# Kernel tuning notes

Measured on AMD Instinct MI355X. Metric: run time of the kernel, lower is better.

## Reference

```python
import jax, jax.numpy as jnp
import numpy as np

LEN_HIS = 20   # q_len_his: sliding-window history length
DIM_C = 4      # dim_c
H = 64         # GRU hidden = final_mlp_hidden_width
D = 36         # global_graph_width(32) + goal(2) + action(2)
N = 32768      # total timesteps across many episodes


def setup_inputs() -> dict:
    key = jax.random.key(0)
    ks = jax.random.split(key, 8)
    emb = jax.random.normal(ks[0], (N, D), jnp.float32)
    dones = (jax.random.uniform(ks[1], (N, 1)) < 0.02).astype(jnp.int32)
    s = lambda k, shape, fan: jax.random.normal(k, shape, jnp.float32) / np.sqrt(fan).astype(np.float32)
    return {
        "embeddings": emb,
        "W_ih": s(ks[2], (3 * H, D), D),
        "W_hh": s(ks[3], (3 * H, H), H),
        "b_ih": jnp.zeros((3 * H,), jnp.float32),
        "b_hh": jnp.zeros((3 * H,), jnp.float32),
        "W1": s(ks[4], (H, H), H),
        "b1": jnp.zeros((H,), jnp.float32),
        "W2": s(ks[5], (DIM_C, H), H),
        "b2": jnp.zeros((DIM_C,), jnp.float32),
        "dones": dones,
    }


def _his_calculate_c(embeddings, W_ih, W_hh, b_ih, b_hh, W1, b1, W2, b2, dones):
    """Batched/padded version of the ragged sliding-window GRU+MLP loop.

    For each timestep t, the torch code runs the GRU over
    embeddings[max(episode_start, t-L+1) : t+1] from a zero hidden state,
    then applies FinalPredMLP to the final hidden state.
    """
    n = embeddings.shape[0]
    done = dones[:, 0] != 0
    idx = jnp.arange(n)
    # episode_start[t] = (index of most recent done strictly before t) + 1, else 0
    prev_done = jnp.concatenate([jnp.zeros((1,), bool), done[:-1]])
    ep_start = jax.lax.cummax(jnp.where(prev_done, idx, 0))
    win_start = jnp.maximum(ep_start, idx - LEN_HIS + 1)            # [N]

    # padded windows: position l holds embeddings[t - (L-1) + l]
    gidx = idx[:, None] - (LEN_HIS - 1) + jnp.arange(LEN_HIS)[None, :]  # [N, L]
    valid = gidx >= win_start[:, None]                                   # [N, L]
    X = embeddings[jnp.clip(gidx, 0, n - 1)] * valid[..., None]          # [N, L, D]

    def cell(h, inp):
        x, v = inp                      # x: [N, D], v: [N]
        gi = x @ W_ih.T + b_ih          # [N, 3H]
        gh = h @ W_hh.T + b_hh          # [N, 3H]
        ir, iz, inn = jnp.split(gi, 3, axis=-1)
        hr, hz, hnn = jnp.split(gh, 3, axis=-1)
        r = jax.nn.sigmoid(ir + hr)
        z = jax.nn.sigmoid(iz + hz)
        ncand = jnp.tanh(inn + r * hnn)
        h_new = (1.0 - z) * ncand + z * h
        return jnp.where(v[:, None], h_new, h), None

    h0 = jnp.zeros((n, H), embeddings.dtype)
    hT, _ = jax.lax.scan(cell, h0, (jnp.swapaxes(X, 0, 1), valid.T))  # [N, H]

    # FinalPredMLP: Linear(H,H) -> ReLU -> Linear(H, dim_c)
    hid = jax.nn.relu(hT @ W1.T + b1)
    return hid @ W2.T + b2              # [N, dim_c]


def reference(embeddings, W_ih, W_hh, b_ih, b_hh, W1, b1, W2, b2, dones):
    return _his_calculate_c(embeddings, W_ih, W_hh, b_ih, b_hh, W1, b1, W2, b2, dones)
```

## Files before the change

kernel.cpp:

```cpp
#include <hip/hip_runtime.h>

#define NT 32768
#define DI 36
#define HH 64
#define G3 192
#define LH 20
#define SGS 196

#define NLOG2E -1.4426950408889634f
#define TLOG2E 2.8853900817779268f

#define UNION_OFF  27440
#define SFIRST_OFF 32480
#define SMEM_BYTES 32544

typedef __attribute__((ext_vector_type(8))) short bf16x8;
typedef __attribute__((ext_vector_type(4))) float f32x4;
typedef __attribute__((ext_vector_type(4))) int int4v;
union frag_cast { int4v i4; bf16x8 h8; };

__device__ __forceinline__ unsigned f2u(float f) { union { float f; unsigned u; } x; x.f = f; return x.u; }
__device__ __forceinline__ float u2f(unsigned u) { union { float f; unsigned u; } x; x.u = u; return x.f; }
__device__ __forceinline__ unsigned short f2bf_rne(float f) {
    union { float f; unsigned u; } x; x.f = f;
    unsigned r = x.u + 0x7FFFu + ((x.u >> 16) & 1u);
    return (unsigned short)(r >> 16);
}

__global__ __launch_bounds__(64) void prep_kernel(
    const float* __restrict__ W_ih, const float* __restrict__ W_hh,
    const float* __restrict__ W1, int4v* __restrict__ wfrag)
{
    const int b = (int)blockIdx.x;
    const int l = (int)threadIdx.x;
    unsigned short e[8];
    if (b < 72) {
        const int set = b / 24, fb = b % 24;
        const int mt = fb >> 1, kt = fb & 1;
        const int m = mt * 16 + (l & 15);
        const float sc = ((mt >> 2) < 2) ? NLOG2E : TLOG2E;
        const int k0 = kt * 32 + (l >> 4) * 8;
#pragma unroll
        for (int jj = 0; jj < 8; ++jj) {
            const int k = k0 + jj;
            if (set == 2) {
                e[jj] = f2bf_rne(W_hh[(size_t)m * HH + k] * sc);
            } else {
                const float v = (k < DI) ? W_ih[(size_t)m * DI + k] * sc : 0.f;
                const unsigned u = f2u(v);
                if (set == 0) e[jj] = (unsigned short)(u >> 16);
                else          e[jj] = (unsigned short)(f2u(v - u2f(u & 0xFFFF0000u)) >> 16);
            }
        }
    } else {
        const int bb = b - 72;
        const bool is_lo = bb >= 8;
        const int f = bb & 7;
        const int mt = f >> 1, kt = f & 1;
        const int m = mt * 16 + (l & 15);
        const int k0 = kt * 32 + (l >> 4) * 8;
#pragma unroll
        for (int jj = 0; jj < 8; ++jj) {
            const float v = W1[(size_t)m * HH + k0 + jj];
            const unsigned u = f2u(v);
            if (!is_lo) e[jj] = (unsigned short)(u >> 16);
            else        e[jj] = (unsigned short)(f2u(v - u2f(u & 0xFFFF0000u)) >> 16);
        }
    }
    int4v p;
    p.x = e[0] | ((unsigned)e[1] << 16); p.y = e[2] | ((unsigned)e[3] << 16);
    p.z = e[4] | ((unsigned)e[5] << 16); p.w = e[6] | ((unsigned)e[7] << 16);
    wfrag[b * 64 + l] = p;
}

__global__ __launch_bounds__(256, 5) void gru_kernel(
    const float* __restrict__ emb, const int4v* __restrict__ wfrag,
    const float* __restrict__ b_ih, const float* __restrict__ b_hh,
    const float* __restrict__ b1, const float* __restrict__ W2,
    const float* __restrict__ b2, const int* __restrict__ dones,
    float* __restrict__ out)
{
    __shared__ __align__(16) char SMEM[SMEM_BYTES];
    float* const Sg = (float*)SMEM;
    unsigned short* const EmbP = (unsigned short*)(SMEM + UNION_OFF);
    unsigned short* const HbB  = (unsigned short*)(SMEM + UNION_OFF);
    unsigned short* const HfH  = (unsigned short*)(SMEM + UNION_OFF);
    unsigned short* const HfL  = HfH + 1152;
    int* const sfirst = (int*)(SMEM + SFIRST_OFF);

    const int tid = threadIdx.x;
    const int lane = tid & 63;
    const int W = tid >> 6;
    const int li = lane & 15;
    const int q = lane >> 4;
    const int blk = ((int)blockIdx.x & 7) * 256 + ((int)blockIdx.x >> 3);
    const int T0 = blk * 16;

    float ev[5];
#pragma unroll
    for (int k = 0; k < 5; ++k) {
        const int i = tid + 256 * k;
        if (i < 35 * DI) {
            const int r = i / DI, c = i % DI;
            int tt = T0 - (LH - 1) + r; tt = tt < 0 ? 0 : tt;
            ev[k] = emb[(size_t)tt * DI + c];
        }
    }
    {
        int4v* z = (int4v*)EmbP;
        for (int i = tid; i < 315; i += 256) z[i] = int4v{0, 0, 0, 0};
    }
    if (tid < 16) {
        const int tt = T0 + tid;
        int lo = tt - (LH - 1); if (lo < 0) lo = 0;
        int ws = lo;
        for (int j = lo; j < tt; ++j)
            ws = (dones[j] != 0) ? (j + 1) : ws;
        sfirst[tid] = ws - (tt - (LH - 1));
    }
    __syncthreads();
#pragma unroll
    for (int k = 0; k < 5; ++k) {
        const int i = tid + 256 * k;
        if (i < 35 * DI)
            EmbP[(i / DI) * 72 + (i % DI)] = (unsigned short)(f2u(ev[k]) >> 16);
    }

    bf16x8 aih[3][2], ail[3][2];
#pragma unroll
    for (int g = 0; g < 3; ++g)
#pragma unroll
        for (int kt = 0; kt < 2; ++kt) {
            const int fb = (4 * g + W) * 2 + kt;
            frag_cast a, b;
            a.i4 = wfrag[(0 * 24 + fb) * 64 + lane];
            b.i4 = wfrag[(1 * 24 + fb) * 64 + lane];
            aih[g][kt] = a.h8; ail[g][kt] = b.h8;
        }

    const int joff = 16 * W + 4 * q;
    f32x4 biasI[3];
#pragma unroll
    for (int g = 0; g < 3; ++g) {
        const float sc = (g < 2) ? NLOG2E : TLOG2E;
        const f32x4 bi = *(const f32x4*)&b_ih[64 * g + joff];
        if (g < 2) {
            const f32x4 bh = *(const f32x4*)&b_hh[64 * g + joff];
#pragma unroll
            for (int rr = 0; rr < 4; ++rr) biasI[g][rr] = (bi[rr] + bh[rr]) * sc;
        } else {
#pragma unroll
            for (int rr = 0; rr < 4; ++rr) biasI[g][rr] = bi[rr] * sc;
        }
    }
    __syncthreads();

#pragma unroll
    for (int nt = 0; nt < 3; ++nt) {
        const int row = 16 * nt + li;
        const int rowr = row < 35 ? row : 34;
        bf16x8 ebh[2];
#pragma unroll
        for (int kt = 0; kt < 2; ++kt)
            ebh[kt] = *(const bf16x8*)&EmbP[rowr * 72 + 32 * kt + 8 * q];
#pragma unroll
        for (int g = 0; g < 3; ++g) {
            f32x4 a = biasI[g];
            a = __builtin_amdgcn_mfma_f32_16x16x32_bf16(aih[g][0], ebh[0], a, 0, 0, 0);
            a = __builtin_amdgcn_mfma_f32_16x16x32_bf16(aih[g][1], ebh[1], a, 0, 0, 0);
            a = __builtin_amdgcn_mfma_f32_16x16x32_bf16(ail[g][0], ebh[0], a, 0, 0, 0);
            a = __builtin_amdgcn_mfma_f32_16x16x32_bf16(ail[g][1], ebh[1], a, 0, 0, 0);
            if (row < 35)
                *(f32x4*)&Sg[row * SGS + 64 * g + joff] = a;
        }
    }
    __syncthreads();
#pragma unroll
    for (int k = 0; k < 5; ++k) {
        const int i = tid + 256 * k;
        if (i < 35 * DI) {
            const unsigned u = f2u(ev[k]);
            EmbP[(i / DI) * 72 + (i % DI)] =
                (unsigned short)(f2u(ev[k] - u2f(u & 0xFFFF0000u)) >> 16);
        }
    }
    __syncthreads();

#pragma unroll
    for (int nt = 0; nt < 3; ++nt) {
        const int row = 16 * nt + li;
        const int rowr = row < 35 ? row : 34;
        bf16x8 ebl[2];
#pragma unroll
        for (int kt = 0; kt < 2; ++kt)
            ebl[kt] = *(const bf16x8*)&EmbP[rowr * 72 + 32 * kt + 8 * q];
#pragma unroll
        for (int g = 0; g < 3; ++g) {
            f32x4 a = *(const f32x4*)&Sg[rowr * SGS + 64 * g + joff];
            a = __builtin_amdgcn_mfma_f32_16x16x32_bf16(aih[g][0], ebl[0], a, 0, 0, 0);
            a = __builtin_amdgcn_mfma_f32_16x16x32_bf16(aih[g][1], ebl[1], a, 0, 0, 0);
            if (row < 35)
                *(f32x4*)&Sg[row * SGS + 64 * g + joff] = a;
        }
    }
    __syncthreads();
    const int sfr = sfirst[li];

    bf16x8 whh[3][2];
#pragma unroll
    for (int g = 0; g < 3; ++g)
#pragma unroll
        for (int kt = 0; kt < 2; ++kt) {
            frag_cast c; c.i4 = wfrag[(48 + (4 * g + W) * 2 + kt) * 64 + lane];
            whh[g][kt] = c.h8;
        }
    f32x4 bnv;
    {
        const f32x4 b = *(const f32x4*)&b_hh[128 + joff];
#pragma unroll
        for (int rr = 0; rr < 4; ++rr) bnv[rr] = b[rr] * TLOG2E;
    }

    float h[4] = {0.f, 0.f, 0.f, 0.f};
    f32x4 accR, accZ, accN, ginv;
    f32x4 gvR, gvZ, gvN;

    {
        const float* gp = Sg + li * SGS;
        accR = *(const f32x4*)(gp + joff);
        accZ = *(const f32x4*)(gp + 64 + joff);
        ginv = *(const f32x4*)(gp + 128 + joff);
        accN = bnv;
        const bool valid = (0 >= sfr);
#pragma unroll
        for (int rr = 0; rr < 4; ++rr) {
            const float r  = __builtin_amdgcn_rcpf(1.f + __builtin_amdgcn_exp2f(accR[rr]));
            const float z  = __builtin_amdgcn_rcpf(1.f + __builtin_amdgcn_exp2f(accZ[rr]));
            const float nc = 1.f - 2.f * __builtin_amdgcn_rcpf(1.f + __builtin_amdgcn_exp2f(ginv[rr] + r * accN[rr]));
            h[rr] = valid ? fmaf(z, 0.f - nc, nc) : 0.f;
        }
        uint2 ph;
        ph.x = __builtin_amdgcn_perm(f2u(h[1]), f2u(h[0]), 0x07060302u);
        ph.y = __builtin_amdgcn_perm(f2u(h[3]), f2u(h[2]), 0x07060302u);
        *(uint2*)&HbB[1152 + li * 72 + joff] = ph;
        const float* gq = Sg + (li + 1) * SGS;
        gvR = *(const f32x4*)(gq + joff);
        gvZ = *(const f32x4*)(gq + 64 + joff);
        gvN = *(const f32x4*)(gq + 128 + joff);
    }
    __syncthreads();

#pragma unroll 2
    for (int s = 1; s < LH; ++s) {
        const int rb = s & 1;
        const bf16x8 bh0 = *(const bf16x8*)&HbB[rb * 1152 + li * 72 + 8 * q];
        const bf16x8 bh1 = *(const bf16x8*)&HbB[rb * 1152 + li * 72 + 32 + 8 * q];

        accR = gvR; accZ = gvZ; ginv = gvN; accN = bnv;
        {
            int r = li + s + 1; r = r > 34 ? 34 : r;
            const float* gq = Sg + r * SGS;
            gvR = *(const f32x4*)(gq + joff);
            gvZ = *(const f32x4*)(gq + 64 + joff);
            gvN = *(const f32x4*)(gq + 128 + joff);
        }
#pragma unroll
        for (int g = 0; g < 3; ++g) {
            f32x4 a = (g == 0) ? accR : (g == 1) ? accZ : accN;
            a = __builtin_amdgcn_mfma_f32_16x16x32_bf16(whh[g][0], bh0, a, 0, 0, 0);
            a = __builtin_amdgcn_mfma_f32_16x16x32_bf16(whh[g][1], bh1, a, 0, 0, 0);
            if (g == 0) accR = a; else if (g == 1) accZ = a; else accN = a;
        }
        const bool valid = (s >= sfr);
#pragma unroll
        for (int rr = 0; rr < 4; ++rr) {
            const float r  = __builtin_amdgcn_rcpf(1.f + __builtin_amdgcn_exp2f(accR[rr]));
            const float z  = __builtin_amdgcn_rcpf(1.f + __builtin_amdgcn_exp2f(accZ[rr]));
            const float nc = 1.f - 2.f * __builtin_amdgcn_rcpf(1.f + __builtin_amdgcn_exp2f(ginv[rr] + r * accN[rr]));
            const float hn = fmaf(z, h[rr] - nc, nc);
            h[rr] = valid ? hn : h[rr];
        }
        if (s != LH - 1) {
            uint2 ph;
            ph.x = __builtin_amdgcn_perm(f2u(h[1]), f2u(h[0]), 0x07060302u);
            ph.y = __builtin_amdgcn_perm(f2u(h[3]), f2u(h[2]), 0x07060302u);
            *(uint2*)&HbB[(1 - rb) * 1152 + li * 72 + joff] = ph;
        }
        __syncthreads();
    }

    {
        const unsigned u0 = f2u(h[0]), u1 = f2u(h[1]);
        const unsigned u2 = f2u(h[2]), u3 = f2u(h[3]);
        uint2 ph, pl;
        ph.x = __builtin_amdgcn_perm(u1, u0, 0x07060302u);
        ph.y = __builtin_amdgcn_perm(u3, u2, 0x07060302u);
        const unsigned l0 = f2u(h[0] - u2f(u0 & 0xFFFF0000u));
        const unsigned l1 = f2u(h[1] - u2f(u1 & 0xFFFF0000u));
        const unsigned l2 = f2u(h[2] - u2f(u2 & 0xFFFF0000u));
        const unsigned l3 = f2u(h[3] - u2f(u3 & 0xFFFF0000u));
        pl.x = __builtin_amdgcn_perm(l1, l0, 0x07060302u);
        pl.y = __builtin_amdgcn_perm(l3, l2, 0x07060302u);
        *(uint2*)&HfH[li * 72 + joff] = ph;
        *(uint2*)&HfL[li * 72 + joff] = pl;
    }
    __syncthreads();
    {
        bf16x8 w1h[2], w1l[2];
#pragma unroll
        for (int kt = 0; kt < 2; ++kt) {
            frag_cast a, b;
            a.i4 = wfrag[(72 + W * 2 + kt) * 64 + lane];
            b.i4 = wfrag[(80 + W * 2 + kt) * 64 + lane];
            w1h[kt] = a.h8; w1l[kt] = b.h8;
        }
        const bf16x8 bh0 = *(const bf16x8*)&HfH[li * 72 + 8 * q];
        const bf16x8 bh1 = *(const bf16x8*)&HfH[li * 72 + 32 + 8 * q];
        const bf16x8 bl0 = *(const bf16x8*)&HfL[li * 72 + 8 * q];
        const bf16x8 bl1 = *(const bf16x8*)&HfL[li * 72 + 32 + 8 * q];
        f32x4 a = *(const f32x4*)&b1[joff];
        a = __builtin_amdgcn_mfma_f32_16x16x32_bf16(w1h[0], bh0, a, 0, 0, 0);
        a = __builtin_amdgcn_mfma_f32_16x16x32_bf16(w1h[1], bh1, a, 0, 0, 0);
        a = __builtin_amdgcn_mfma_f32_16x16x32_bf16(w1l[0], bh0, a, 0, 0, 0);
        a = __builtin_amdgcn_mfma_f32_16x16x32_bf16(w1l[1], bh1, a, 0, 0, 0);
        a = __builtin_amdgcn_mfma_f32_16x16x32_bf16(w1h[0], bl0, a, 0, 0, 0);
        a = __builtin_amdgcn_mfma_f32_16x16x32_bf16(w1h[1], bl1, a, 0, 0, 0);
        __syncthreads();
        float4 st;
        st.x = fmaxf(a[0], 0.f); st.y = fmaxf(a[1], 0.f);
        st.z = fmaxf(a[2], 0.f); st.w = fmaxf(a[3], 0.f);
        *(float4*)&Sg[li * 68 + joff] = st;
    }
    __syncthreads();
    if (tid < 64) {
        const int tt = tid >> 2, c = tid & 3;
        float o2 = b2[c];
        for (int m4 = 0; m4 < 16; ++m4) {
            const float4 hv = *(const float4*)&Sg[tt * 68 + 4 * m4];
            const float4 wv = *(const float4*)&W2[c * HH + 4 * m4];
            o2 += hv.x * wv.x + hv.y * wv.y + hv.z * wv.z + hv.w * wv.w;
        }
        out[(size_t)(T0 + tt) * 4 + c] = o2;
    }
}

extern "C" void kernel_launch(void* const* d_in, const int* in_sizes, int n_in,
                              void* d_out, int out_size, void* d_ws, size_t ws_size,
                              hipStream_t stream) {
    const float* emb  = (const float*)d_in[0];
    const float* W_ih = (const float*)d_in[1];
    const float* W_hh = (const float*)d_in[2];
    const float* b_ih = (const float*)d_in[3];
    const float* b_hh = (const float*)d_in[4];
    const float* W1   = (const float*)d_in[5];
    const float* b1   = (const float*)d_in[6];
    const float* W2   = (const float*)d_in[7];
    const float* b2   = (const float*)d_in[8];
    const int*   dn   = (const int*)d_in[9];

    int4v* wfrag = (int4v*)d_ws;
    float* o = (float*)d_out;

    prep_kernel<<<88, 64, 0, stream>>>(W_ih, W_hh, W1, wfrag);
    gru_kernel<<<NT / 16, 256, 0, stream>>>(emb, wfrag, b_ih, b_hh,
                                            b1, W2, b2, dn, o);
}
```

Before: 116.9 us.

## Store input-gate preactivations as fp16 in LDS and merge embedding split passes

```diff
diff --git a/kernel.cpp b/kernel.cpp
--- a/kernel.cpp
+++ b/kernel.cpp
@@ -1,18 +1,19 @@
 #include <hip/hip_runtime.h>
+#include <hip/hip_fp16.h>
 
 #define NT 32768
 #define DI 36
 #define HH 64
 #define G3 192
 #define LH 20
-#define SGS 196
+#define SGH 200
 
 #define NLOG2E -1.4426950408889634f
 #define TLOG2E 2.8853900817779268f
 
-#define UNION_OFF  27440
-#define SFIRST_OFF 32480
-#define SMEM_BYTES 32544
+#define UNION_OFF  14000
+#define SFIRST_OFF 24080
+#define SMEM_BYTES 24144
 
 typedef __attribute__((ext_vector_type(8))) short bf16x8;
 typedef __attribute__((ext_vector_type(4))) float f32x4;
@@ -25,6 +26,17 @@
     union { float f; unsigned u; } x; x.f = f;
     unsigned r = x.u + 0x7FFFu + ((x.u >> 16) & 1u);
     return (unsigned short)(r >> 16);
+}
+__device__ __forceinline__ f32x4 h4f(uint2 p) {
+    const __half2* a = (const __half2*)&p;
+    const float2 f0 = __half22float2(a[0]);
+    const float2 f1 = __half22float2(a[1]);
+    f32x4 r; r[0] = f0.x; r[1] = f0.y; r[2] = f1.x; r[3] = f1.y; return r;
+}
+__device__ __forceinline__ uint2 f4h(f32x4 v) {
+    __half2 h0 = __floats2half2_rn(v[0], v[1]);
+    __half2 h1 = __floats2half2_rn(v[2], v[3]);
+    uint2 r; r.x = *(unsigned*)&h0; r.y = *(unsigned*)&h1; return r;
 }
 
 __global__ __launch_bounds__(64) void prep_kernel(
@@ -73,7 +85,7 @@
     wfrag[b * 64 + l] = p;
 }
 
-__global__ __launch_bounds__(256, 5) void gru_kernel(
+__global__ __launch_bounds__(256, 6) void gru_kernel(
     const float* __restrict__ emb, const int4v* __restrict__ wfrag,
     const float* __restrict__ b_ih, const float* __restrict__ b_hh,
     const float* __restrict__ b1, const float* __restrict__ W2,
@@ -81,8 +93,9 @@
     float* __restrict__ out)
 {
     __shared__ __align__(16) char SMEM[SMEM_BYTES];
-    float* const Sg = (float*)SMEM;
-    unsigned short* const EmbP = (unsigned short*)(SMEM + UNION_OFF);
+    unsigned short* const Sg = (unsigned short*)SMEM;
+    unsigned short* const EmbH = (unsigned short*)(SMEM + UNION_OFF);
+    unsigned short* const EmbL = EmbH + 35 * 72;
     unsigned short* const HbB  = (unsigned short*)(SMEM + UNION_OFF);
     unsigned short* const HfH  = (unsigned short*)(SMEM + UNION_OFF);
     unsigned short* const HfL  = HfH + 1152;
@@ -107,8 +120,8 @@
         }
     }
     {
-        int4v* z = (int4v*)EmbP;
-        for (int i = tid; i < 315; i += 256) z[i] = int4v{0, 0, 0, 0};
+        int4v* z = (int4v*)EmbH;
+        for (int i = tid; i < 630; i += 256) z[i] = int4v{0, 0, 0, 0};
     }
     if (tid < 16) {
         const int tt = T0 + tid;
@@ -122,8 +135,12 @@
 #pragma unroll
     for (int k = 0; k < 5; ++k) {
         const int i = tid + 256 * k;
-        if (i < 35 * DI)
-            EmbP[(i / DI) * 72 + (i % DI)] = (unsigned short)(f2u(ev[k]) >> 16);
+        if (i < 35 * DI) {
+            const int idx = (i / DI) * 72 + (i % DI);
+            const unsigned u = f2u(ev[k]);
+            EmbH[idx] = (unsigned short)(u >> 16);
+            EmbL[idx] = (unsigned short)(f2u(ev[k] - u2f(u & 0xFFFF0000u)) >> 16);
+        }
     }
 
     bf16x8 aih[3][2], ail[3][2];
@@ -159,10 +176,12 @@
     for (int nt = 0; nt < 3; ++nt) {
         const int row = 16 * nt + li;
         const int rowr = row < 35 ? row : 34;
-        bf16x8 ebh[2];
-#pragma unroll
-        for (int kt = 0; kt < 2; ++kt)
-            ebh[kt] = *(const bf16x8*)&EmbP[rowr * 72 + 32 * kt + 8 * q];
+        bf16x8 ebh[2], ebl[2];
+#pragma unroll
+        for (int kt = 0; kt < 2; ++kt) {
+            ebh[kt] = *(const bf16x8*)&EmbH[rowr * 72 + 32 * kt + 8 * q];
+            ebl[kt] = *(const bf16x8*)&EmbL[rowr * 72 + 32 * kt + 8 * q];
+        }
 #pragma unroll
         for (int g = 0; g < 3; ++g) {
             f32x4 a = biasI[g];
@@ -170,37 +189,10 @@
             a = __builtin_amdgcn_mfma_f32_16x16x32_bf16(aih[g][1], ebh[1], a, 0, 0, 0);
             a = __builtin_amdgcn_mfma_f32_16x16x32_bf16(ail[g][0], ebh[0], a, 0, 0, 0);
             a = __builtin_amdgcn_mfma_f32_16x16x32_bf16(ail[g][1], ebh[1], a, 0, 0, 0);
-            if (row < 35)
-                *(f32x4*)&Sg[row * SGS + 64 * g + joff] = a;
-        }
-    }
-    __syncthreads();
-#pragma unroll
-    for (int k = 0; k < 5; ++k) {
-        const int i = tid + 256 * k;
-        if (i < 35 * DI) {
-            const unsigned u = f2u(ev[k]);
-            EmbP[(i / DI) * 72 + (i % DI)] =
-                (unsigned short)(f2u(ev[k] - u2f(u & 0xFFFF0000u)) >> 16);
-        }
-    }
-    __syncthreads();
-
-#pragma unroll
-    for (int nt = 0; nt < 3; ++nt) {
-        const int row = 16 * nt + li;
-        const int rowr = row < 35 ? row : 34;
-        bf16x8 ebl[2];
-#pragma unroll
-        for (int kt = 0; kt < 2; ++kt)
-            ebl[kt] = *(const bf16x8*)&EmbP[rowr * 72 + 32 * kt + 8 * q];
-#pragma unroll
-        for (int g = 0; g < 3; ++g) {
-            f32x4 a = *(const f32x4*)&Sg[rowr * SGS + 64 * g + joff];
             a = __builtin_amdgcn_mfma_f32_16x16x32_bf16(aih[g][0], ebl[0], a, 0, 0, 0);
             a = __builtin_amdgcn_mfma_f32_16x16x32_bf16(aih[g][1], ebl[1], a, 0, 0, 0);
             if (row < 35)
-                *(f32x4*)&Sg[row * SGS + 64 * g + joff] = a;
+                *(uint2*)&Sg[row * SGH + 64 * g + joff] = f4h(a);
         }
     }
     __syncthreads();
@@ -223,13 +215,12 @@
 
     float h[4] = {0.f, 0.f, 0.f, 0.f};
     f32x4 accR, accZ, accN, ginv;
-    f32x4 gvR, gvZ, gvN;
-
-    {
-        const float* gp = Sg + li * SGS;
-        accR = *(const f32x4*)(gp + joff);
-        accZ = *(const f32x4*)(gp + 64 + joff);
-        ginv = *(const f32x4*)(gp + 128 + joff);
+    uint2 pR, pZ, pN;
+
+    {
+        accR = h4f(*(const uint2*)&Sg[li * SGH + joff]);
+        accZ = h4f(*(const uint2*)&Sg[li * SGH + 64 + joff]);
+        ginv = h4f(*(const uint2*)&Sg[li * SGH + 128 + joff]);
         accN = bnv;
         const bool valid = (0 >= sfr);
 #pragma unroll
@@ -243,10 +234,9 @@
         ph.x = __builtin_amdgcn_perm(f2u(h[1]), f2u(h[0]), 0x07060302u);
         ph.y = __builtin_amdgcn_perm(f2u(h[3]), f2u(h[2]), 0x07060302u);
         *(uint2*)&HbB[1152 + li * 72 + joff] = ph;
-        const float* gq = Sg + (li + 1) * SGS;
-        gvR = *(const f32x4*)(gq + joff);
-        gvZ = *(const f32x4*)(gq + 64 + joff);
-        gvN = *(const f32x4*)(gq + 128 + joff);
+        pR = *(const uint2*)&Sg[(li + 1) * SGH + joff];
+        pZ = *(const uint2*)&Sg[(li + 1) * SGH + 64 + joff];
+        pN = *(const uint2*)&Sg[(li + 1) * SGH + 128 + joff];
     }
     __syncthreads();
 
@@ -256,13 +246,12 @@
         const bf16x8 bh0 = *(const bf16x8*)&HbB[rb * 1152 + li * 72 + 8 * q];
         const bf16x8 bh1 = *(const bf16x8*)&HbB[rb * 1152 + li * 72 + 32 + 8 * q];
 
-        accR = gvR; accZ = gvZ; ginv = gvN; accN = bnv;
+        accR = h4f(pR); accZ = h4f(pZ); ginv = h4f(pN); accN = bnv;
         {
             int r = li + s + 1; r = r > 34 ? 34 : r;
-            const float* gq = Sg + r * SGS;
-            gvR = *(const f32x4*)(gq + joff);
-            gvZ = *(const f32x4*)(gq + 64 + joff);
-            gvN = *(const f32x4*)(gq + 128 + joff);
+            pR = *(const uint2*)&Sg[r * SGH + joff];
+            pZ = *(const uint2*)&Sg[r * SGH + 64 + joff];
+            pN = *(const uint2*)&Sg[r * SGH + 128 + joff];
         }
 #pragma unroll
         for (int g = 0; g < 3; ++g) {
@@ -305,6 +294,7 @@
         *(uint2*)&HfL[li * 72 + joff] = pl;
     }
     __syncthreads();
+    float* const Hid = (float*)SMEM;
     {
         bf16x8 w1h[2], w1l[2];
 #pragma unroll
@@ -329,14 +319,14 @@
         float4 st;
         st.x = fmaxf(a[0], 0.f); st.y = fmaxf(a[1], 0.f);
         st.z = fmaxf(a[2], 0.f); st.w = fmaxf(a[3], 0.f);
-        *(float4*)&Sg[li * 68 + joff] = st;
+        *(float4*)&Hid[li * 68 + joff] = st;
     }
     __syncthreads();
     if (tid < 64) {
         const int tt = tid >> 2, c = tid & 3;
         float o2 = b2[c];
         for (int m4 = 0; m4 < 16; ++m4) {
-            const float4 hv = *(const float4*)&Sg[tt * 68 + 4 * m4];
+            const float4 hv = *(const float4*)&Hid[tt * 68 + 4 * m4];
             const float4 wv = *(const float4*)&W2[c * HH + 4 * m4];
             o2 += hv.x * wv.x + hv.y * wv.y + hv.z * wv.z + hv.w * wv.w;
         }
```

Measured after the change: 145.5 us. 1.24x slower.
